# Optimization experiments

Measured on AMD Instinct MI355X. Metric: run time of the kernel, lower is better.

Reference implementation:

```python
import jax, jax.numpy as jnp
import numpy as np
from jax import lax


def lstm(x, W, U, b):
    """Keras-style LSTM, return_sequences=True, zero init state.
    x: [B,T,I], W: [I,4H], U: [H,4H], b: [4H]. Gate order i,f,g,o."""
    B, T, _ = x.shape
    H = U.shape[0]
    # precompute input contribution for all timesteps: [T,B,4H]
    xz = jnp.swapaxes(jnp.einsum('bti,ij->btj', x, W) + b, 0, 1)

    def step(carry, xz_t):
        h, c = carry
        z = xz_t + h @ U  # [B,4H]
        i, f, g, o = jnp.split(z, 4, axis=-1)
        i = jax.nn.sigmoid(i)
        f = jax.nn.sigmoid(f)
        g = jnp.tanh(g)
        o = jax.nn.sigmoid(o)
        c = f * c + i * g
        h = o * jnp.tanh(c)
        return (h, c), h

    h0 = jnp.zeros((B, H), x.dtype)
    _, hs = lax.scan(step, (h0, h0), xz)
    return jnp.swapaxes(hs, 0, 1)  # [B,T,H]


def setup_inputs() -> dict:
    key = jax.random.key(0)
    B, T, L, H = 2048, 64, 64, 1024
    G = 4 * H
    ks = jax.random.split(key, 16)
    s = 0.05  # small init scale to avoid gate saturation
    return {
        'x':    jax.random.normal(ks[0], (B, T, L), jnp.float32),
        'g1_W': jax.random.normal(ks[1], (L, G), jnp.float32) * s,
        'g1_U': jax.random.normal(ks[2], (H, G), jnp.float32) * s,
        'g1_b': jnp.zeros((G,), jnp.float32),
        'g2_W': jax.random.normal(ks[3], (H, G), jnp.float32) * s,
        'g2_U': jax.random.normal(ks[4], (H, G), jnp.float32) * s,
        'g2_b': jnp.zeros((G,), jnp.float32),
        'g3_W': jax.random.normal(ks[5], (H, 4), jnp.float32) * s,
        'g3_U': jax.random.normal(ks[6], (1, 4), jnp.float32) * s,
        'g3_b': jnp.zeros((4,), jnp.float32),
        'd1_W': jax.random.normal(ks[7], (1, G), jnp.float32) * s,
        'd1_U': jax.random.normal(ks[8], (H, G), jnp.float32) * s,
        'd1_b': jnp.zeros((G,), jnp.float32),
        'd2_W': jax.random.normal(ks[9], (H, G), jnp.float32) * s,
        'd2_U': jax.random.normal(ks[10], (H, G), jnp.float32) * s,
        'd2_b': jnp.zeros((G,), jnp.float32),
        'do_W': jax.random.normal(ks[11], (H, 1), jnp.float32) * s,
        'do_b': jnp.zeros((1,), jnp.float32),
    }


def reference(x, g1_W, g1_U, g1_b, g2_W, g2_U, g2_b, g3_W, g3_U, g3_b,
              d1_W, d1_U, d1_b, d2_W, d2_U, d2_b, do_W, do_b):
    # generator: LSTM(H) -> LSTM(H) -> LSTM(1)  (training=False => dropout inactive)
    h = lstm(x, g1_W, g1_U, g1_b)
    h = lstm(h, g2_W, g2_U, g2_b)
    gen = lstm(h, g3_W, g3_U, g3_b)            # [B,T,1]
    # discriminator: LSTM(H) -> LSTM(H) -> Dense(1)
    d = lstm(gen, d1_W, d1_U, d1_b)
    d = lstm(d, d2_W, d2_U, d2_b)
    disc = d @ do_W + do_b                      # [B,T,1]
    return gen, disc
```

## Files before the change

kernel.cpp:

```cpp
#include <hip/hip_runtime.h>

typedef unsigned short u16;
typedef __attribute__((ext_vector_type(8))) short short8;
typedef __attribute__((ext_vector_type(4))) float f32x4;

#define B_ 2048
#define T_ 64
#define I_ 64
#define H_ 1024
#define G_ 4096

__device__ __forceinline__ float bf2f(u16 v) {
  union { float f; unsigned u; } x; x.u = ((unsigned)v) << 16; return x.f;
}
__device__ __forceinline__ u16 f2bf(float f) {
  union { float f; unsigned u; } x; x.f = f;
  unsigned r = x.u + 0x7fffu + ((x.u >> 16) & 1u);
  return (u16)(r >> 16);
}
__device__ __forceinline__ float sigm(float x) { return 1.0f / (1.0f + __expf(-x)); }
__device__ __forceinline__ float tanh_(float x) { return 1.0f - 2.0f / (__expf(2.0f * x) + 1.0f); }



__global__ void k_transpose_x(const float* __restrict__ x, u16* __restrict__ xT) {
  int idx = blockIdx.x * 256 + threadIdx.x;
  if (idx >= B_ * T_ * I_) return;
  int i = idx & 63;
  int t = (idx >> 6) & 63;
  int b = idx >> 12;
  size_t dst = (size_t)t * B_ * I_ +
               ((size_t)((b >> 4) * 8 + (i >> 3)) << 7) + ((b & 15) << 3) + (i & 7);
  xT[dst] = f2bf(x[idx]);
}

__global__ void k_build_bt(const float* __restrict__ U, const float* __restrict__ W,
                           u16* __restrict__ BT, int K0, int K) {
  int n = blockIdx.y;
  int k = blockIdx.x * 256 + threadIdx.x;
  if (k >= K) return;
  int j = (n & 3) * 1024 + (n >> 2);
  float v = (k < K0) ? U[(size_t)k * G_ + j] : W[(size_t)(k - K0) * G_ + j];
  BT[(size_t)n * K + k] = f2bf(v);
}

__global__ void k_build_bias(const float* __restrict__ b1, const float* __restrict__ b2,
                             const float* __restrict__ bd1, const float* __restrict__ bd2,
                             const float* __restrict__ d1W,
                             float* __restrict__ p1, float* __restrict__ p2,
                             float* __restrict__ pd1, float* __restrict__ pd2,
                             float* __restrict__ pd1W) {
  int n = blockIdx.x * 256 + threadIdx.x;
  if (n >= G_) return;
  int j = (n & 3) * 1024 + (n >> 2);
  p1[n] = b1[j]; p2[n] = b2[j]; pd1[n] = bd1[j]; pd2[n] = bd2[j];
  pd1W[n] = d1W[j];
}


struct GemmP {
  const u16* A0; int ka0, kt0;
  const u16* A1; int ka1, kt1;
  const u16* BT; int ldb;
  const float* biasp;
  const float* evec;
  const float* escal; int estride;
  float* cst; u16* hout;
};


#define LOADB(kt_, tb) do {                                                   \
    int kk_ = (kt_);                                                          \
    _Pragma("unroll")                                                         \
    for (int s = 0; s < 4; ++s) tb[s] = *(const short8*)(pB[s] + (size_t)kk_ * 64); \
  } while (0)

#define WRITEB(tb, SOFF) do {                                                 \
    _Pragma("unroll")                                                         \
    for (int s = 0; s < 4; ++s) *(short8*)&smem[(SOFF) + wpos[s]] = tb[s];    \
  } while (0)

#define LOADA(kt_, fa) do {                                                   \
    int kk_ = (kt_);                                                          \
    if (kk_ < p.kt0) {                                                        \
      size_t o_ = (size_t)kk_ * 1024;                                         \
      _Pragma("unroll")                                                       \
      for (int i = 0; i < 4; ++i) {                                           \
        fa[i * 2] = *(const short8*)(baseA0[i] + o_);                         \
        fa[i * 2 + 1] = *(const short8*)(baseA0[i] + o_ + 512);               \
      }                                                                       \
    } else {                                                                  \
      size_t o_ = (size_t)(kk_ - p.kt0) * 1024;                               \
      _Pragma("unroll")                                                       \
      for (int i = 0; i < 4; ++i) {                                           \
        fa[i * 2] = *(const short8*)(baseA1[i] + o_);                         \
        fa[i * 2 + 1] = *(const short8*)(baseA1[i] + o_ + 512);               \
      }                                                                       \
    }                                                                         \
  } while (0)

#define COMPUTET(SOFF, fa) do {                                               \
    __builtin_amdgcn_s_setprio(1);                                            \
    _Pragma("unroll")                                                         \
    for (int ks = 0; ks < 2; ++ks) {                                          \
      const int sw = ((((ks << 2) + q) ^ l7) << 3);                           \
      short8 bfv[4];                                                          \
      _Pragma("unroll")                                                       \
      for (int j = 0; j < 4; ++j) bfv[j] = *(const short8*)&smem[(SOFF) + boffr[j] + sw]; \
      _Pragma("unroll")                                                       \
      for (int i = 0; i < 4; ++i)                                             \
        _Pragma("unroll")                                                     \
        for (int j = 0; j < 4; ++j)                                           \
          acc[i][j] = __builtin_amdgcn_mfma_f32_16x16x32_bf16(fa[i * 2 + ks], bfv[j], acc[i][j], 0, 0, 0); \
    }                                                                         \
    __builtin_amdgcn_s_setprio(0);                                            \
  } while (0)

#define KBAR() do {                                                           \
    asm volatile("s_waitcnt lgkmcnt(0)" ::: "memory");                        \
    __builtin_amdgcn_s_barrier();                                             \
  } while (0)

__device__ __forceinline__ void gemm_body(u16* smem, const GemmP& p, int m0, int n0) {
  const int tid = threadIdx.x;
  const int lane = tid & 63;
  const int w = tid >> 6;
  const int KT = p.kt0 + p.kt1;

  const int wm = (w >> 1) << 6, wn = (w & 1) << 6;
  const int q = lane >> 4, l15 = lane & 15, l7 = lane & 7;

  const int r_ = tid >> 3, c_ = tid & 7;
  const u16* pB[4];
  int wpos[4];
#pragma unroll
  for (int s = 0; s < 4; ++s) {
    int rs = (s << 5) + r_;
    pB[s] = p.BT + (size_t)(n0 + rs) * p.ldb + (c_ << 3);
    wpos[s] = (rs << 6) + ((c_ ^ (rs & 7)) << 3);
  }

  const int mb4 = (m0 + wm) >> 4;
  const int K80 = p.ka0 >> 3;
  const int K81 = p.A1 ? (p.ka1 >> 3) : K80;
  const u16* baseA0[4]; const u16* baseA1[4];
#pragma unroll
  for (int i = 0; i < 4; ++i) {
    baseA0[i] = p.A0 + (((size_t)(mb4 + i) * K80 + q) << 7) + (l15 << 3);
    baseA1[i] = p.A1 ? (p.A1 + (((size_t)(mb4 + i) * K81 + q) << 7) + (l15 << 3))
                     : baseA0[i];
  }

  f32x4 acc[4][4];
#pragma unroll
  for (int i = 0; i < 4; ++i)
#pragma unroll
    for (int j = 0; j < 4; ++j) acc[i][j] = (f32x4){0.f, 0.f, 0.f, 0.f};

  int boffr[4];
#pragma unroll
  for (int i = 0; i < 4; ++i) boffr[i] = (wn + (i << 4) + l15) << 6;

  short8 afA[8], afB[8], sb0[4], sb1[4];

  LOADB(0, sb0);
  LOADB(1, sb1);
  LOADA(0, afA);
  WRITEB(sb0, 0);
  KBAR();

  for (int kt = 0; kt < KT; kt += 2) {
    if (kt + 1 < KT) LOADA(kt + 1, afB);
    if (kt + 2 < KT) LOADB(kt + 2, sb0);
    if (kt + 1 < KT) WRITEB(sb1, 8192);
    COMPUTET(0, afA);
    KBAR();
    if (kt + 1 >= KT) break;
    if (kt + 2 < KT) LOADA(kt + 2, afA);
    if (kt + 3 < KT) LOADB(kt + 3, sb1);
    if (kt + 2 < KT) WRITEB(sb0, 0);
    COMPUTET(8192, afB);
    KBAR();
  }

  __syncthreads();
  float* ep = (float*)smem + w * 1280;
  const int ul = lane & 3, ml = lane >> 2;
  const int ubase = (n0 >> 2) + (wn >> 2);
#pragma unroll 1
  for (int tj = 0; tj < 4; ++tj) {
#pragma unroll
    for (int ti = 0; ti < 4; ++ti)
#pragma unroll
      for (int v = 0; v < 4; ++v)
        ep[((ti << 4) + (q << 2) + v) * 20 + l15] = acc[ti][tj][v];
    __syncthreads();
#pragma unroll
    for (int pp = 0; pp < 4; ++pp) {
      int row = ml + (pp << 4);
      f32x4 z = *(const f32x4*)&ep[row * 20 + (ul << 2)];
      int gm = m0 + wm + row;
      int gu = ubase + (tj << 2) + ul;
      const f32x4 bb = *(const f32x4*)&p.biasp[gu << 2];
      z.x += bb.x; z.y += bb.y; z.z += bb.z; z.w += bb.w;
      if (p.evec) {
        float gs = p.escal[(size_t)gm * p.estride];
        const f32x4 ev = *(const f32x4*)&p.evec[gu << 2];
        z.x += gs * ev.x; z.y += gs * ev.y; z.z += gs * ev.z; z.w += gs * ev.w;
      }
      float ig = sigm(z.x), fg = sigm(z.y), gg = tanh_(z.z), og = sigm(z.w);
      size_t ci = ((size_t)gm << 10) + gu;
      float cn = fg * p.cst[ci] + ig * gg;
      p.cst[ci] = cn;
      size_t hi = ((size_t)((gm >> 4) * 128 + (gu >> 3)) << 7) + ((gm & 15) << 3) + (gu & 7);
      p.hout[hi] = f2bf(og * tanh_(cn));
    }
    __syncthreads();
  }
}

__global__ __launch_bounds__(256, 2) void k_gemm(GemmP p) {
  __shared__ u16 smem[16384];
  int id = blockIdx.y * 16 + blockIdx.x;
  int xcd = id & 7, slot = id >> 3;
  int by = (xcd << 2) + (slot >> 4);
  int bx = slot & 15;
  gemm_body(smem, p, bx << 7, by << 7);
}

__global__ __launch_bounds__(256, 2) void k_gemm2(GemmP pa, GemmP pb) {
  __shared__ u16 smem[16384];
  int id = blockIdx.y * 32 + blockIdx.x;
  int xcd = id & 7, slot = id >> 3;
  const GemmP& p = (xcd & 1) ? pb : pa;
  int by = ((xcd >> 1) << 3) + (slot >> 4);
  int bx = slot & 15;
  gemm_body(smem, p, bx << 7, by << 7);
}


__global__ void k_g3(const u16* __restrict__ h2, const float* __restrict__ W,
                     const float* __restrict__ Uv, const float* __restrict__ bv,
                     float* __restrict__ c3, float* __restrict__ h3,
                     float* __restrict__ gen, int t) {
  int b = blockIdx.x * 4 + (threadIdx.x >> 6);
  int lane = threadIdx.x & 63;
  float a0 = 0.f, a1 = 0.f, a2 = 0.f, a3 = 0.f;
  for (int ch = lane; ch < 128; ch += 64) {
    short8 v = *(const short8*)&h2[((size_t)((b >> 4) * 128 + ch) << 7) + ((b & 15) << 3)];
#pragma unroll
    for (int e = 0; e < 8; ++e) {
      float hv = bf2f((u16)v[e]);
      const f32x4 wv = *(const f32x4*)&W[(ch * 8 + e) << 2];
      a0 += hv * wv.x; a1 += hv * wv.y; a2 += hv * wv.z; a3 += hv * wv.w;
    }
  }
  for (int off = 32; off; off >>= 1) {
    a0 += __shfl_down(a0, off);
    a1 += __shfl_down(a1, off);
    a2 += __shfl_down(a2, off);
    a3 += __shfl_down(a3, off);
  }
  if (lane == 0) {
    float hp = h3[b];
    float zi = a0 + hp * Uv[0] + bv[0];
    float zf = a1 + hp * Uv[1] + bv[1];
    float zg = a2 + hp * Uv[2] + bv[2];
    float zo = a3 + hp * Uv[3] + bv[3];
    float cn = sigm(zf) * c3[b] + sigm(zi) * tanh_(zg);
    c3[b] = cn;
    float hn = sigm(zo) * tanh_(cn);
    h3[b] = hn;
    gen[b * T_ + t] = hn;
  }
}

__global__ void k_dense(const u16* __restrict__ hd2, const float* __restrict__ wv,
                        const float* __restrict__ bs, float* __restrict__ disc, int t) {
  int b = blockIdx.x * 4 + (threadIdx.x >> 6);
  int lane = threadIdx.x & 63;
  float a = 0.f;
  for (int ch = lane; ch < 128; ch += 64) {
    short8 v = *(const short8*)&hd2[((size_t)((b >> 4) * 128 + ch) << 7) + ((b & 15) << 3)];
#pragma unroll
    for (int e = 0; e < 8; ++e) a += bf2f((u16)v[e]) * wv[ch * 8 + e];
  }
  for (int off = 32; off; off >>= 1) a += __shfl_down(a, off);
  if (lane == 0) disc[b * T_ + t] = a + bs[0];
}

__global__ void k_small(const u16* __restrict__ h2s, const float* __restrict__ W,
                        const float* __restrict__ Uv, const float* __restrict__ bv,
                        float* __restrict__ c3, float* __restrict__ h3,
                        float* __restrict__ gen, int tg,
                        const u16* __restrict__ hd2s, const float* __restrict__ wv,
                        const float* __restrict__ bs, float* __restrict__ disc, int td) {
  int lane = threadIdx.x & 63;
  if (blockIdx.x < 512) {
    int b = blockIdx.x * 4 + (threadIdx.x >> 6);
    float a0 = 0.f, a1 = 0.f, a2 = 0.f, a3 = 0.f;
    for (int ch = lane; ch < 128; ch += 64) {
      short8 v = *(const short8*)&h2s[((size_t)((b >> 4) * 128 + ch) << 7) + ((b & 15) << 3)];
#pragma unroll
      for (int e = 0; e < 8; ++e) {
        float hv = bf2f((u16)v[e]);
        const f32x4 wv4 = *(const f32x4*)&W[(ch * 8 + e) << 2];
        a0 += hv * wv4.x; a1 += hv * wv4.y; a2 += hv * wv4.z; a3 += hv * wv4.w;
      }
    }
    for (int off = 32; off; off >>= 1) {
      a0 += __shfl_down(a0, off);
      a1 += __shfl_down(a1, off);
      a2 += __shfl_down(a2, off);
      a3 += __shfl_down(a3, off);
    }
    if (lane == 0) {
      float hp = h3[b];
      float zi = a0 + hp * Uv[0] + bv[0];
      float zf = a1 + hp * Uv[1] + bv[1];
      float zg = a2 + hp * Uv[2] + bv[2];
      float zo = a3 + hp * Uv[3] + bv[3];
      float cn = sigm(zf) * c3[b] + sigm(zi) * tanh_(zg);
      c3[b] = cn;
      float hn = sigm(zo) * tanh_(cn);
      h3[b] = hn;
      gen[b * T_ + tg] = hn;
    }
  } else {
    int b = (blockIdx.x - 512) * 4 + (threadIdx.x >> 6);
    float a = 0.f;
    for (int ch = lane; ch < 128; ch += 64) {
      short8 v = *(const short8*)&hd2s[((size_t)((b >> 4) * 128 + ch) << 7) + ((b & 15) << 3)];
#pragma unroll
      for (int e = 0; e < 8; ++e) a += bf2f((u16)v[e]) * wv[ch * 8 + e];
    }
    for (int off = 32; off; off >>= 1) a += __shfl_down(a, off);
    if (lane == 0) disc[b * T_ + td] = a + bs[0];
  }
}


extern "C" void kernel_launch(void* const* d_in, const int* in_sizes, int n_in,
                              void* d_out, int out_size, void* d_ws, size_t ws_size,
                              hipStream_t stream) {
  const float* x   = (const float*)d_in[0];
  const float* g1W = (const float*)d_in[1];
  const float* g1U = (const float*)d_in[2];
  const float* g1b = (const float*)d_in[3];
  const float* g2W = (const float*)d_in[4];
  const float* g2U = (const float*)d_in[5];
  const float* g2b = (const float*)d_in[6];
  const float* g3W = (const float*)d_in[7];
  const float* g3U = (const float*)d_in[8];
  const float* g3b = (const float*)d_in[9];
  const float* d1W = (const float*)d_in[10];
  const float* d1U = (const float*)d_in[11];
  const float* d1b = (const float*)d_in[12];
  const float* d2W = (const float*)d_in[13];
  const float* d2U = (const float*)d_in[14];
  const float* d2b = (const float*)d_in[15];
  const float* doW = (const float*)d_in[16];
  const float* dob = (const float*)d_in[17];

  char* ws = (char*)d_ws;
  u16* xT    = (u16*)(ws + 0);
  u16* BT1   = (u16*)(ws + 16777216);
  u16* BT2   = (u16*)(ws + 25690112);
  u16* BTd1  = (u16*)(ws + 42467328);
  u16* BTd2  = (u16*)(ws + 50855936);
  float* pb1  = (float*)(ws + 67633152);
  float* pb2  = (float*)(ws + 67649536);
  float* pbd1 = (float*)(ws + 67665920);
  float* pbd2 = (float*)(ws + 67682304);
  float* pd1W = (float*)(ws + 67698688);
  const size_t Z0 = 67715072;
  float* c1  = (float*)(ws + Z0);
  float* c2  = (float*)(ws + Z0 + 8388608);
  float* cd1 = (float*)(ws + Z0 + 16777216);
  float* cd2 = (float*)(ws + Z0 + 25165824);
  u16* h1[2]  = {(u16*)(ws + Z0 + 33554432), (u16*)(ws + Z0 + 37748736)};
  u16* h2[2]  = {(u16*)(ws + Z0 + 41943040), (u16*)(ws + Z0 + 46137344)};
  u16* hd1[2] = {(u16*)(ws + Z0 + 50331648), (u16*)(ws + Z0 + 54525952)};
  u16* hd2[2] = {(u16*)(ws + Z0 + 58720256), (u16*)(ws + Z0 + 62914560)};
  float* c3 = (float*)(ws + Z0 + 67108864);
  float* h3 = (float*)(ws + Z0 + 67117056);
  const size_t ZBYTES = 67125248;

  k_transpose_x<<<32768, 256, 0, stream>>>(x, xT);
  k_build_bt<<<dim3(5, 4096), 256, 0, stream>>>(g1U, g1W, BT1, 1024, 1088);
  k_build_bt<<<dim3(8, 4096), 256, 0, stream>>>(g2U, g2W, BT2, 1024, 2048);
  k_build_bt<<<dim3(4, 4096), 256, 0, stream>>>(d1U, nullptr, BTd1, 1024, 1024);
  k_build_bt<<<dim3(8, 4096), 256, 0, stream>>>(d2U, d2W, BTd2, 1024, 2048);
  k_build_bias<<<16, 256, 0, stream>>>(g1b, g2b, d1b, d2b, d1W, pb1, pb2, pbd1, pbd2, pd1W);
  (void)hipMemsetAsync(ws + Z0, 0, ZBYTES, stream);

  float* gen = (float*)d_out;
  float* disc = gen + (size_t)B_ * T_;
  dim3 blk(256);
  dim3 grid1(16, 32), grid2(32, 32);

  {
    GemmP pg1 = {h1[0], H_, 16, xT, I_, 1, BT1, 1088,
                 pb1, nullptr, nullptr, 0, c1, h1[1]};
    k_gemm<<<grid1, blk, 0, stream>>>(pg1);
    GemmP pg2 = {h2[0], H_, 16, h1[1], H_, 16, BT2, 2048,
                 pb2, nullptr, nullptr, 0, c2, h2[1]};
    k_gemm<<<grid1, blk, 0, stream>>>(pg2);
    k_g3<<<512, blk, 0, stream>>>(h2[1], g3W, g3U, g3b, c3, h3, gen, 0);
  }

  for (int t = 0; t < 63; ++t) {
    int rg = (t + 1) & 1, wg = rg ^ 1;
    int rd = t & 1, wd = rd ^ 1;
    GemmP pg1 = {h1[rg], H_, 16, xT + (size_t)(t + 1) * B_ * I_, I_, 1, BT1, 1088,
                 pb1, nullptr, nullptr, 0, c1, h1[wg]};
    GemmP pd1 = {hd1[rd], H_, 16, nullptr, 0, 0, BTd1, 1024,
                 pbd1, pd1W, gen + t, T_, cd1, hd1[wd]};
    k_gemm2<<<grid2, blk, 0, stream>>>(pg1, pd1);
    GemmP pg2 = {h2[rg], H_, 16, h1[wg], H_, 16, BT2, 2048,
                 pb2, nullptr, nullptr, 0, c2, h2[wg]};
    GemmP pd2 = {hd2[rd], H_, 16, hd1[wd], H_, 16, BTd2, 2048,
                 pbd2, nullptr, nullptr, 0, cd2, hd2[wd]};
    k_gemm2<<<grid2, blk, 0, stream>>>(pg2, pd2);
    k_small<<<1024, blk, 0, stream>>>(h2[wg], g3W, g3U, g3b, c3, h3, gen, t + 1,
                                      hd2[wd], doW, dob, disc, t);
  }

  {
    GemmP pd1 = {hd1[1], H_, 16, nullptr, 0, 0, BTd1, 1024,
                 pbd1, pd1W, gen + 63, T_, cd1, hd1[0]};
    k_gemm<<<grid1, blk, 0, stream>>>(pd1);
    GemmP pd2 = {hd2[1], H_, 16, hd1[0], H_, 16, BTd2, 2048,
                 pbd2, nullptr, nullptr, 0, cd2, hd2[0]};
    k_gemm<<<grid1, blk, 0, stream>>>(pd2);
    k_dense<<<512, blk, 0, stream>>>(hd2[0], doW, dob, disc, 63);
  }
  (void)in_sizes; (void)n_in; (void)out_size; (void)ws_size;
}
```

Baseline: 13.35 ms.

## Use 8-wave blocks with smaller per-wave tiles and templated GEMM dimensions

Blocks grow from 4 to 8 waves on the same 128x128 tile, so each wave now owns a 64x32 sub-tile instead of 64x64. This halves the accumulator and B-fragment registers and allows more waves in flight. K extents, leading dimension and A-stride become template parameters, removing runtime branches and address arithmetic. The A-fragment double buffer is dropped, so A loads now happen right before compute with less latency hiding, and B-tile reuse per wave is lower.

```diff
diff --git a/kernel.cpp b/kernel.cpp
--- a/kernel.cpp
+++ b/kernel.cpp
@@ -59,9 +59,9 @@
 
 
 struct GemmP {
-  const u16* A0; int ka0, kt0;
-  const u16* A1; int ka1, kt1;
-  const u16* BT; int ldb;
+  const u16* A0;
+  const u16* A1;
+  const u16* BT;
   const float* biasp;
   const float* evec;
   const float* escal; int estride;
@@ -69,126 +69,123 @@
 };
 
 
-#define LOADB(kt_, tb) do {                                                   \
-    int kk_ = (kt_);                                                          \
-    _Pragma("unroll")                                                         \
-    for (int s = 0; s < 4; ++s) tb[s] = *(const short8*)(pB[s] + (size_t)kk_ * 64); \
-  } while (0)
-
-#define WRITEB(tb, SOFF) do {                                                 \
-    _Pragma("unroll")                                                         \
-    for (int s = 0; s < 4; ++s) *(short8*)&smem[(SOFF) + wpos[s]] = tb[s];    \
-  } while (0)
-
-#define LOADA(kt_, fa) do {                                                   \
-    int kk_ = (kt_);                                                          \
-    if (kk_ < p.kt0) {                                                        \
-      size_t o_ = (size_t)kk_ * 1024;                                         \
-      _Pragma("unroll")                                                       \
-      for (int i = 0; i < 4; ++i) {                                           \
-        fa[i * 2] = *(const short8*)(baseA0[i] + o_);                         \
-        fa[i * 2 + 1] = *(const short8*)(baseA0[i] + o_ + 512);               \
-      }                                                                       \
-    } else {                                                                  \
-      size_t o_ = (size_t)(kk_ - p.kt0) * 1024;                               \
-      _Pragma("unroll")                                                       \
-      for (int i = 0; i < 4; ++i) {                                           \
-        fa[i * 2] = *(const short8*)(baseA1[i] + o_);                         \
-        fa[i * 2 + 1] = *(const short8*)(baseA1[i] + o_ + 512);               \
-      }                                                                       \
-    }                                                                         \
-  } while (0)
-
-#define COMPUTET(SOFF, fa) do {                                               \
-    __builtin_amdgcn_s_setprio(1);                                            \
-    _Pragma("unroll")                                                         \
-    for (int ks = 0; ks < 2; ++ks) {                                          \
-      const int sw = ((((ks << 2) + q) ^ l7) << 3);                           \
-      short8 bfv[4];                                                          \
-      _Pragma("unroll")                                                       \
-      for (int j = 0; j < 4; ++j) bfv[j] = *(const short8*)&smem[(SOFF) + boffr[j] + sw]; \
-      _Pragma("unroll")                                                       \
-      for (int i = 0; i < 4; ++i)                                             \
-        _Pragma("unroll")                                                     \
-        for (int j = 0; j < 4; ++j)                                           \
-          acc[i][j] = __builtin_amdgcn_mfma_f32_16x16x32_bf16(fa[i * 2 + ks], bfv[j], acc[i][j], 0, 0, 0); \
-    }                                                                         \
-    __builtin_amdgcn_s_setprio(0);                                            \
-  } while (0)
-
 #define KBAR() do {                                                           \
     asm volatile("s_waitcnt lgkmcnt(0)" ::: "memory");                        \
     __builtin_amdgcn_s_barrier();                                             \
   } while (0)
 
+template<int LDB, int KT0, int KT1, int K81>
 __device__ __forceinline__ void gemm_body(u16* smem, const GemmP& p, int m0, int n0) {
   const int tid = threadIdx.x;
   const int lane = tid & 63;
   const int w = tid >> 6;
-  const int KT = p.kt0 + p.kt1;
-
-  const int wm = (w >> 1) << 6, wn = (w & 1) << 6;
+  constexpr int KT = KT0 + KT1;
+
+  const int wm = (w >> 2) << 6;
+  const int wn = (w & 3) << 5;
   const int q = lane >> 4, l15 = lane & 15, l7 = lane & 7;
 
   const int r_ = tid >> 3, c_ = tid & 7;
-  const u16* pB[4];
-  int wpos[4];
-#pragma unroll
-  for (int s = 0; s < 4; ++s) {
-    int rs = (s << 5) + r_;
-    pB[s] = p.BT + (size_t)(n0 + rs) * p.ldb + (c_ << 3);
+  const u16* pB[2];
+  int wpos[2];
+#pragma unroll
+  for (int s = 0; s < 2; ++s) {
+    int rs = (s << 6) + r_;
+    pB[s] = p.BT + (size_t)(n0 + rs) * LDB + (c_ << 3);
     wpos[s] = (rs << 6) + ((c_ ^ (rs & 7)) << 3);
   }
 
   const int mb4 = (m0 + wm) >> 4;
-  const int K80 = p.ka0 >> 3;
-  const int K81 = p.A1 ? (p.ka1 >> 3) : K80;
-  const u16* baseA0[4]; const u16* baseA1[4];
+  const u16* baseA0[4];
+  const u16* baseA1[4];
 #pragma unroll
   for (int i = 0; i < 4; ++i) {
-    baseA0[i] = p.A0 + (((size_t)(mb4 + i) * K80 + q) << 7) + (l15 << 3);
-    baseA1[i] = p.A1 ? (p.A1 + (((size_t)(mb4 + i) * K81 + q) << 7) + (l15 << 3))
-                     : baseA0[i];
-  }
-
-  f32x4 acc[4][4];
+    baseA0[i] = p.A0 + (((size_t)(mb4 + i) * 128 + q) << 7) + (l15 << 3);
+    if constexpr (KT1 > 0)
+      baseA1[i] = p.A1 + (((size_t)(mb4 + i) * K81 + q) << 7) + (l15 << 3);
+    else
+      baseA1[i] = nullptr;
+  }
+
+  f32x4 acc[4][2];
 #pragma unroll
   for (int i = 0; i < 4; ++i)
 #pragma unroll
-    for (int j = 0; j < 4; ++j) acc[i][j] = (f32x4){0.f, 0.f, 0.f, 0.f};
-
-  int boffr[4];
-#pragma unroll
-  for (int i = 0; i < 4; ++i) boffr[i] = (wn + (i << 4) + l15) << 6;
-
-  short8 afA[8], afB[8], sb0[4], sb1[4];
-
-  LOADB(0, sb0);
-  LOADB(1, sb1);
-  LOADA(0, afA);
-  WRITEB(sb0, 0);
+    for (int j = 0; j < 2; ++j) acc[i][j] = (f32x4){0.f, 0.f, 0.f, 0.f};
+
+  int boffr[2];
+#pragma unroll
+  for (int j = 0; j < 2; ++j) boffr[j] = (wn + (j << 4) + l15) << 6;
+
+  short8 af[8], tb0[2], tb1[2];
+
+  auto loadB = [&](int kk, short8* tb) {
+#pragma unroll
+    for (int s = 0; s < 2; ++s) tb[s] = *(const short8*)(pB[s] + (size_t)kk * 64);
+  };
+  auto writeB = [&](short8* tb, int soff) {
+#pragma unroll
+    for (int s = 0; s < 2; ++s) *(short8*)&smem[soff + wpos[s]] = tb[s];
+  };
+  auto loadA = [&](int kk) {
+    if (KT1 == 0 || kk < KT0) {
+      size_t o = (size_t)kk * 1024;
+#pragma unroll
+      for (int i = 0; i < 4; ++i) {
+        af[i * 2] = *(const short8*)(baseA0[i] + o);
+        af[i * 2 + 1] = *(const short8*)(baseA0[i] + o + 512);
+      }
+    } else {
+      size_t o = (size_t)(kk - KT0) * 1024;
+#pragma unroll
+      for (int i = 0; i < 4; ++i) {
+        af[i * 2] = *(const short8*)(baseA1[i] + o);
+        af[i * 2 + 1] = *(const short8*)(baseA1[i] + o + 512);
+      }
+    }
+  };
+  auto compute = [&](int soff) {
+    __builtin_amdgcn_s_setprio(1);
+#pragma unroll
+    for (int ks = 0; ks < 2; ++ks) {
+      const int sw = ((((ks << 2) + q) ^ l7) << 3);
+      short8 bfv[2];
+#pragma unroll
+      for (int j = 0; j < 2; ++j) bfv[j] = *(const short8*)&smem[soff + boffr[j] + sw];
+#pragma unroll
+      for (int i = 0; i < 4; ++i)
+#pragma unroll
+        for (int j = 0; j < 2; ++j)
+          acc[i][j] = __builtin_amdgcn_mfma_f32_16x16x32_bf16(af[i * 2 + ks], bfv[j], acc[i][j], 0, 0, 0);
+    }
+    __builtin_amdgcn_s_setprio(0);
+  };
+
+  loadB(0, tb0);
+  loadB(1, tb1);
+  writeB(tb0, 0);
   KBAR();
 
   for (int kt = 0; kt < KT; kt += 2) {
-    if (kt + 1 < KT) LOADA(kt + 1, afB);
-    if (kt + 2 < KT) LOADB(kt + 2, sb0);
-    if (kt + 1 < KT) WRITEB(sb1, 8192);
-    COMPUTET(0, afA);
+    loadA(kt);
+    if (kt + 2 < KT) loadB(kt + 2, tb0);
+    if (kt + 1 < KT) writeB(tb1, 8192);
+    compute(0);
     KBAR();
     if (kt + 1 >= KT) break;
-    if (kt + 2 < KT) LOADA(kt + 2, afA);
-    if (kt + 3 < KT) LOADB(kt + 3, sb1);
-    if (kt + 2 < KT) WRITEB(sb0, 0);
-    COMPUTET(8192, afB);
+    loadA(kt + 1);
+    if (kt + 3 < KT) loadB(kt + 3, tb1);
+    if (kt + 2 < KT) writeB(tb0, 0);
+    compute(8192);
     KBAR();
   }
 
   __syncthreads();
   float* ep = (float*)smem + w * 1280;
   const int ul = lane & 3, ml = lane >> 2;
-  const int ubase = (n0 >> 2) + (wn >> 2);
+  const int ubase = (n0 >> 2) + ((w & 3) << 3);
 #pragma unroll 1
-  for (int tj = 0; tj < 4; ++tj) {
+  for (int tj = 0; tj < 2; ++tj) {
 #pragma unroll
     for (int ti = 0; ti < 4; ++ti)
 #pragma unroll
@@ -219,23 +216,26 @@
   }
 }
 
-__global__ __launch_bounds__(256, 2) void k_gemm(GemmP p) {
-  __shared__ u16 smem[16384];
+template<int LDB, int KT0, int KT1, int K81>
+__global__ __launch_bounds__(512, 4) void k_gemm(GemmP p) {
+  __shared__ u16 smem[20480];
   int id = blockIdx.y * 16 + blockIdx.x;
   int xcd = id & 7, slot = id >> 3;
   int by = (xcd << 2) + (slot >> 4);
   int bx = slot & 15;
-  gemm_body(smem, p, bx << 7, by << 7);
-}
-
-__global__ __launch_bounds__(256, 2) void k_gemm2(GemmP pa, GemmP pb) {
-  __shared__ u16 smem[16384];
+  gemm_body<LDB, KT0, KT1, K81>(smem, p, bx << 7, by << 7);
+}
+
+template<int LDBa, int KT0a, int KT1a, int K81a,
+         int LDBb, int KT0b, int KT1b, int K81b>
+__global__ __launch_bounds__(512, 4) void k_gemm2(GemmP pa, GemmP pb) {
+  __shared__ u16 smem[20480];
   int id = blockIdx.y * 32 + blockIdx.x;
   int xcd = id & 7, slot = id >> 3;
-  const GemmP& p = (xcd & 1) ? pb : pa;
   int by = ((xcd >> 1) << 3) + (slot >> 4);
   int bx = slot & 15;
-  gemm_body(smem, p, bx << 7, by << 7);
+  if (xcd & 1) gemm_body<LDBb, KT0b, KT1b, K81b>(smem, pb, bx << 7, by << 7);
+  else         gemm_body<LDBa, KT0a, KT1a, K81a>(smem, pa, bx << 7, by << 7);
 }
 
 
@@ -396,43 +396,37 @@
 
   float* gen = (float*)d_out;
   float* disc = gen + (size_t)B_ * T_;
-  dim3 blk(256);
+  dim3 blk5(512), blk(256);
   dim3 grid1(16, 32), grid2(32, 32);
 
   {
-    GemmP pg1 = {h1[0], H_, 16, xT, I_, 1, BT1, 1088,
-                 pb1, nullptr, nullptr, 0, c1, h1[1]};
-    k_gemm<<<grid1, blk, 0, stream>>>(pg1);
-    GemmP pg2 = {h2[0], H_, 16, h1[1], H_, 16, BT2, 2048,
-                 pb2, nullptr, nullptr, 0, c2, h2[1]};
-    k_gemm<<<grid1, blk, 0, stream>>>(pg2);
+    GemmP pg1 = {h1[0], xT, BT1, pb1, nullptr, nullptr, 0, c1, h1[1]};
+    k_gemm<1088, 16, 1, 8><<<grid1, blk5, 0, stream>>>(pg1);
+    GemmP pg2 = {h2[0], h1[1], BT2, pb2, nullptr, nullptr, 0, c2, h2[1]};
+    k_gemm<2048, 16, 16, 128><<<grid1, blk5, 0, stream>>>(pg2);
     k_g3<<<512, blk, 0, stream>>>(h2[1], g3W, g3U, g3b, c3, h3, gen, 0);
   }
 
   for (int t = 0; t < 63; ++t) {
     int rg = (t + 1) & 1, wg = rg ^ 1;
     int rd = t & 1, wd = rd ^ 1;
-    GemmP pg1 = {h1[rg], H_, 16, xT + (size_t)(t + 1) * B_ * I_, I_, 1, BT1, 1088,
+    GemmP pg1 = {h1[rg], xT + (size_t)(t + 1) * B_ * I_, BT1,
                  pb1, nullptr, nullptr, 0, c1, h1[wg]};
-    GemmP pd1 = {hd1[rd], H_, 16, nullptr, 0, 0, BTd1, 1024,
+    GemmP pd1 = {hd1[rd], nullptr, BTd1,
                  pbd1, pd1W, gen + t, T_, cd1, hd1[wd]};
-    k_gemm2<<<grid2, blk, 0, stream>>>(pg1, pd1);
-    GemmP pg2 = {h2[rg], H_, 16, h1[wg], H_, 16, BT2, 2048,
-                 pb2, nullptr, nullptr, 0, c2, h2[wg]};
-    GemmP pd2 = {hd2[rd], H_, 16, hd1[wd], H_, 16, BTd2, 2048,
-                 pbd2, nullptr, nullptr, 0, cd2, hd2[wd]};
-    k_gemm2<<<grid2, blk, 0, stream>>>(pg2, pd2);
+    k_gemm2<1088, 16, 1, 8, 1024, 16, 0, 0><<<grid2, blk5, 0, stream>>>(pg1, pd1);
+    GemmP pg2 = {h2[rg], h1[wg], BT2, pb2, nullptr, nullptr, 0, c2, h2[wg]};
+    GemmP pd2 = {hd2[rd], hd1[wd], BTd2, pbd2, nullptr, nullptr, 0, cd2, hd2[wd]};
+    k_gemm2<2048, 16, 16, 128, 2048, 16, 16, 128><<<grid2, blk5, 0, stream>>>(pg2, pd2);
     k_small<<<1024, blk, 0, stream>>>(h2[wg], g3W, g3U, g3b, c3, h3, gen, t + 1,
                                       hd2[wd], doW, dob, disc, t);
   }
 
   {
-    GemmP pd1 = {hd1[1], H_, 16, nullptr, 0, 0, BTd1, 1024,
-                 pbd1, pd1W, gen + 63, T_, cd1, hd1[0]};
-    k_gemm<<<grid1, blk, 0, stream>>>(pd1);
-    GemmP pd2 = {hd2[1], H_, 16, hd1[0], H_, 16, BTd2, 2048,
-                 pbd2, nullptr, nullptr, 0, cd2, hd2[0]};
-    k_gemm<<<grid1, blk, 0, stream>>>(pd2);
+    GemmP pd1 = {hd1[1], nullptr, BTd1, pbd1, pd1W, gen + 63, T_, cd1, hd1[0]};
+    k_gemm<1024, 16, 0, 0><<<grid1, blk5, 0, stream>>>(pd1);
+    GemmP pd2 = {hd2[1], hd1[0], BTd2, pbd2, nullptr, nullptr, 0, cd2, hd2[0]};
+    k_gemm<2048, 16, 16, 128><<<grid1, blk5, 0, stream>>>(pd2);
     k_dense<<<512, blk, 0, stream>>>(hd2[0], doW, dob, disc, 63);
   }
   (void)in_sizes; (void)n_in; (void)out_size; (void)ws_size;
```

Result: slower. 14.15 ms (+6.0%).
